# Kernel optimization log

Measured on AMD Instinct MI355X. Metric: run time of the kernel, lower is better.

The kernel has to match this reference:

```python
import jax, jax.numpy as jnp
import numpy as np

B, S, V, D, H, C, NH = 8, 512, 32000, 768, 768, 9, 8
DH = D // NH


def setup_inputs() -> dict:
    key = jax.random.key(0)
    ks = list(jax.random.split(key, 24))
    it = iter(ks)

    def w(shape, s=0.02):
        return jax.random.normal(next(it), shape, jnp.float32) * s

    return {
        "input_ids": jax.random.randint(next(it), (B, S), 0, V, dtype=jnp.int32),
        "labels": jax.random.randint(next(it), (B, S), 0, C, dtype=jnp.int32),
        "emb_table": w((V, D), 1.0),
        "hw_Wh": w((D, D)),
        "hw_bh": jnp.zeros((D,), jnp.float32),
        "hw_Wt": w((D, D)),
        "hw_bt": jnp.zeros((D,), jnp.float32),
        "in_proj_w": w((3 * D, D)),
        "in_proj_b": jnp.zeros((3 * D,), jnp.float32),
        "out_proj_w": w((D, D)),
        "out_proj_b": jnp.zeros((D,), jnp.float32),
        "lstm0_Wih": w((2, 4 * H, D)),
        "lstm0_Whh": w((2, 4 * H, H)),
        "lstm0_b": jnp.zeros((2, 4 * H), jnp.float32),
        "lstm1_Wih": w((2, 4 * H, 2 * H)),
        "lstm1_Whh": w((2, 4 * H, H)),
        "lstm1_b": jnp.zeros((2, 4 * H), jnp.float32),
        "fc_W": w((C, 2 * H)),
        "fc_b": jnp.zeros((C,), jnp.float32),
        "crf_start": w((C,), 0.1),
        "crf_end": w((C,), 0.1),
        "crf_trans": w((C, C), 0.1),
    }


def _lstm_dir(x, Wih, Whh, b, reverse):
    # x: [B,S,in] -> outputs [B,S,H]; PyTorch gate order i,f,g,o
    xt = x.transpose(1, 0, 2)  # [S,B,in]
    h0 = jnp.zeros((x.shape[0], H), x.dtype)

    def step(carry, xt_):
        h, c = carry
        g = xt_ @ Wih.T + h @ Whh.T + b
        i, f, gg, o = jnp.split(g, 4, axis=-1)
        c = jax.nn.sigmoid(f) * c + jax.nn.sigmoid(i) * jnp.tanh(gg)
        h = jax.nn.sigmoid(o) * jnp.tanh(c)
        return (h, c), h

    _, hs = jax.lax.scan(step, (h0, h0), xt, reverse=reverse)
    return hs.transpose(1, 0, 2)


def _bilstm_layer(x, Wih, Whh, b):
    fwd = _lstm_dir(x, Wih[0], Whh[0], b[0], False)
    bwd = _lstm_dir(x, Wih[1], Whh[1], b[1], True)
    return jnp.concatenate([fwd, bwd], axis=-1)


def _emissions(input_ids, emb_table, hw_Wh, hw_bh, hw_Wt, hw_bt,
               in_proj_w, in_proj_b, out_proj_w, out_proj_b,
               lstm0_Wih, lstm0_Whh, lstm0_b, lstm1_Wih, lstm1_Whh, lstm1_b,
               fc_W, fc_b):
    x = emb_table[input_ids]  # [B,S,D]
    # Highway (1 layer, relu)
    hh = jax.nn.relu(x @ hw_Wh.T + hw_bh)
    t = jax.nn.sigmoid(x @ hw_Wt.T + hw_bt)
    x = t * hh + (1.0 - t) * x
    # Multi-head self-attention
    qkv = x @ in_proj_w.T + in_proj_b
    q, k, v = jnp.split(qkv, 3, axis=-1)
    hd = lambda a: a.reshape(B, S, NH, DH).transpose(0, 2, 1, 3)  # [B,NH,S,DH]
    q, k, v = hd(q), hd(k), hd(v)
    att = jax.nn.softmax(jnp.einsum('bhqd,bhkd->bhqk', q, k) / np.float32(np.sqrt(DH)), axis=-1)
    o = jnp.einsum('bhqk,bhkd->bhqd', att, v).transpose(0, 2, 1, 3).reshape(B, S, D)
    x = o @ out_proj_w.T + out_proj_b
    # 2-layer BiLSTM (inference: dropout off)
    x = _bilstm_layer(x, lstm0_Wih, lstm0_Whh, lstm0_b)
    x = _bilstm_layer(x, lstm1_Wih, lstm1_Whh, lstm1_b)
    return x @ fc_W.T + fc_b  # [B,S,C]


def _crf_nll(emissions, tags, crf_start, crf_end, crf_trans):
    # full mask (labels==-100 replaced by 0 before mask built), reduction='sum'
    em_t = emissions.transpose(1, 0, 2)  # [S,B,C]
    num = crf_start[tags[:, 0]] + crf_end[tags[:, -1]]
    num = num + jnp.take_along_axis(emissions, tags[..., None], axis=-1)[..., 0].sum(-1)
    num = num + crf_trans[tags[:, :-1], tags[:, 1:]].sum(-1)
    a0 = crf_start + em_t[0]  # [B,C]

    def fstep(a, em):
        a = jax.scipy.special.logsumexp(a[:, :, None] + crf_trans[None], axis=1) + em
        return a, None

    aT, _ = jax.lax.scan(fstep, a0, em_t[1:])
    logZ = jax.scipy.special.logsumexp(aT + crf_end, axis=-1)
    return -(num - logZ).sum()


def _viterbi(emissions, crf_start, crf_end, crf_trans):
    em_t = emissions.transpose(1, 0, 2)  # [S,B,C]
    s0 = crf_start + em_t[0]

    def vstep(s, em):
        sc = s[:, :, None] + crf_trans[None]  # [B,C_prev,C_next]
        return jnp.max(sc, axis=1) + em, jnp.argmax(sc, axis=1)

    sT, bps = jax.lax.scan(vstep, s0, em_t[1:])  # bps: [S-1,B,C]
    last = jnp.argmax(sT + crf_end, axis=-1)  # [B]

    def bstep(tag, bp):
        prev = jnp.take_along_axis(bp, tag[:, None], axis=1)[:, 0]
        return prev, prev

    _, path = jax.lax.scan(bstep, last, bps, reverse=True)  # [S-1,B]
    return jnp.concatenate([path, last[None]], axis=0).transpose(1, 0)  # [B,S]


def reference(input_ids, labels, emb_table, hw_Wh, hw_bh, hw_Wt, hw_bt,
              in_proj_w, in_proj_b, out_proj_w, out_proj_b,
              lstm0_Wih, lstm0_Whh, lstm0_b, lstm1_Wih, lstm1_Whh, lstm1_b,
              fc_W, fc_b, crf_start, crf_end, crf_trans):
    emissions = _emissions(input_ids, emb_table, hw_Wh, hw_bh, hw_Wt, hw_bt,
                           in_proj_w, in_proj_b, out_proj_w, out_proj_b,
                           lstm0_Wih, lstm0_Whh, lstm0_b,
                           lstm1_Wih, lstm1_Whh, lstm1_b, fc_W, fc_b)
    loss = _crf_nll(emissions, labels, crf_start, crf_end, crf_trans)
    decode = _viterbi(emissions, crf_start, crf_end, crf_trans)
    return loss, decode
```

## Files before the change

kernel.cpp:

```cpp
#include <hip/hip_runtime.h>
#include <cstdint>

#define B_   8
#define S_   512
#define D_   768
#define C_   9
#define BS_  4096

typedef unsigned long long u64;

__global__ __launch_bounds__(192) void k_embed(const int* __restrict__ ids,
                                               const float* __restrict__ emb,
                                               float* __restrict__ x) {
  int row = blockIdx.x;
  int id = ids[row];
  const float4* src = (const float4*)(emb + (size_t)id * D_);
  float4* dst = (float4*)(x + (size_t)row * D_);
  dst[threadIdx.x] = src[threadIdx.x];
}

#define GIDX(k, m) ((k)*144 + (m) + (((m) >> 5) << 2))

__global__ __launch_bounds__(256) void k_gemm(const float* __restrict__ A,
                                              const float* __restrict__ W,
                                              const float* __restrict__ bias,
                                              float* __restrict__ C,
                                              int M, int N, int K, int act, int mode) {
  __shared__ float As[2304];
  __shared__ float Bs[2304];
  int bm0 = blockIdx.y * 128, bn0 = blockIdx.x * 128;
  int tid = threadIdx.x;
  int tm = tid >> 4, tn = tid & 15;
  float acc[8][8];
#pragma unroll
  for (int i = 0; i < 8; ++i)
#pragma unroll
    for (int j = 0; j < 8; ++j) acc[i][j] = 0.f;

  for (int k0 = 0; k0 < K; k0 += 16) {
    __syncthreads();
#pragma unroll
    for (int j = 0; j < 2; ++j) {
      int f4 = tid + j * 256;
      int r = f4 >> 2;
      int kq = (f4 & 3) * 4;
      float4 va = *(const float4*)(A + (size_t)(bm0 + r) * K + k0 + kq);
      As[GIDX(kq + 0, r)] = va.x; As[GIDX(kq + 1, r)] = va.y;
      As[GIDX(kq + 2, r)] = va.z; As[GIDX(kq + 3, r)] = va.w;
      float4 vb = *(const float4*)(W + (size_t)(bn0 + r) * K + k0 + kq);
      Bs[GIDX(kq + 0, r)] = vb.x; Bs[GIDX(kq + 1, r)] = vb.y;
      Bs[GIDX(kq + 2, r)] = vb.z; Bs[GIDX(kq + 3, r)] = vb.w;
    }
    __syncthreads();
#pragma unroll
    for (int kk = 0; kk < 16; ++kk) {
      float a[8], b[8];
      *(float4*)&a[0] = *(const float4*)&As[GIDX(kk, tm * 8)];
      *(float4*)&a[4] = *(const float4*)&As[GIDX(kk, tm * 8 + 4)];
      *(float4*)&b[0] = *(const float4*)&Bs[GIDX(kk, tn * 8)];
      *(float4*)&b[4] = *(const float4*)&Bs[GIDX(kk, tn * 8 + 4)];
#pragma unroll
      for (int i = 0; i < 8; ++i)
#pragma unroll
        for (int j = 0; j < 8; ++j) acc[i][j] += a[i] * b[j];
    }
  }

  float bv[8];
#pragma unroll
  for (int j = 0; j < 8; ++j) bv[j] = bias[bn0 + tn * 8 + j];
#pragma unroll
  for (int i = 0; i < 8; ++i) {
    int row = bm0 + tm * 8 + i;
    float o[8];
#pragma unroll
    for (int j = 0; j < 8; ++j) {
      float v = acc[i][j] + bv[j];
      if (act == 1) v = fmaxf(v, 0.f);
      else if (act == 2) v = 1.f / (1.f + expf(-v));
      o[j] = v;
    }
    if (mode == 0) {
      float* cp = C + (size_t)row * N + bn0 + tn * 8;
      *(float4*)cp = make_float4(o[0], o[1], o[2], o[3]);
      *(float4*)(cp + 4) = make_float4(o[4], o[5], o[6], o[7]);
    } else {
      int bb = row >> 9, t = row & 511;
#pragma unroll
      for (int j = 0; j < 8; ++j) {
        unsigned n = bn0 + tn * 8 + j;
        unsigned dir = n / 3072u;
        unsigned n2 = n - dir * 3072u;
        unsigned g = n2 / 768u;
        unsigned rem = n2 - g * 768u;
        unsigned grp = rem >> 3, u = rem & 7;
        C[(((size_t)(dir * 512 + t) * 96 + grp) << 8) + u * 32 + g * 8 + bb] = o[j];
      }
    }
  }
}

__global__ __launch_bounds__(256) void k_highway(float* __restrict__ x,
                                                 const float* __restrict__ hh,
                                                 const float* __restrict__ tt) {
  const int n4 = BS_ * D_ / 4;
  for (int i = blockIdx.x * 256 + threadIdx.x; i < n4; i += gridDim.x * 256) {
    float4 xv = ((const float4*)x)[i];
    float4 hv = ((const float4*)hh)[i];
    float4 tv = ((const float4*)tt)[i];
    xv.x = tv.x * hv.x + (1.f - tv.x) * xv.x;
    xv.y = tv.y * hv.y + (1.f - tv.y) * xv.y;
    xv.z = tv.z * hv.z + (1.f - tv.z) * xv.z;
    xv.w = tv.w * hv.w + (1.f - tv.w) * xv.w;
    ((float4*)x)[i] = xv;
  }
}

__global__ __launch_bounds__(256) void k_attn(const float* __restrict__ qkv,
                                              float* __restrict__ out) {
  __shared__ float Qs[16 * 100];
  __shared__ float Ks[32 * 101];
  __shared__ float Ps[16 * 513];
  int bh = blockIdx.x;
  int b = bh >> 3, h = bh & 7;
  int q0 = blockIdx.y * 16;
  int tid = threadIdx.x;
  const float scale = 0.10206207261596577f;

  const float* qb = qkv + (size_t)(b * 512 + q0) * 2304 + h * 96;
  for (int i = tid; i < 16 * 96; i += 256) {
    int r = i / 96, c = i - r * 96;
    Qs[r * 100 + c] = qb[(size_t)r * 2304 + c];
  }
  int qi = tid >> 4, kseg = tid & 15;

  for (int kt = 0; kt < 16; ++kt) {
    __syncthreads();
    const float* kb = qkv + (size_t)(b * 512 + kt * 32) * 2304 + 768 + h * 96;
    for (int i = tid; i < 32 * 96; i += 256) {
      int r = i / 96, c = i - r * 96;
      Ks[r * 101 + c] = kb[(size_t)r * 2304 + c];
    }
    __syncthreads();
    int kj0 = kseg * 2;
    float s0 = 0.f, s1 = 0.f;
    const float* qrow = &Qs[qi * 100];
    const float* k0p = &Ks[kj0 * 101];
    const float* k1p = &Ks[(kj0 + 1) * 101];
#pragma unroll 8
    for (int d = 0; d < 96; ++d) {
      float qv = qrow[d];
      s0 += qv * k0p[d];
      s1 += qv * k1p[d];
    }
    Ps[qi * 513 + kt * 32 + kj0] = s0 * scale;
    Ps[qi * 513 + kt * 32 + kj0 + 1] = s1 * scale;
  }
  __syncthreads();

  {
    float m = -1e30f;
    for (int j = 0; j < 32; ++j) m = fmaxf(m, Ps[qi * 513 + kseg + j * 16]);
    m = fmaxf(m, __shfl_xor(m, 1)); m = fmaxf(m, __shfl_xor(m, 2));
    m = fmaxf(m, __shfl_xor(m, 4)); m = fmaxf(m, __shfl_xor(m, 8));
    float sum = 0.f;
    for (int j = 0; j < 32; ++j) {
      int idx = qi * 513 + kseg + j * 16;
      float e = expf(Ps[idx] - m);
      Ps[idx] = e;
      sum += e;
    }
    sum += __shfl_xor(sum, 1); sum += __shfl_xor(sum, 2);
    sum += __shfl_xor(sum, 4); sum += __shfl_xor(sum, 8);
    float inv = 1.f / sum;
    for (int j = 0; j < 32; ++j) Ps[qi * 513 + kseg + j * 16] *= inv;
  }

  float acc[6] = {0.f, 0.f, 0.f, 0.f, 0.f, 0.f};
  int d0 = kseg * 6;
  for (int kt = 0; kt < 16; ++kt) {
    __syncthreads();
    const float* vb = qkv + (size_t)(b * 512 + kt * 32) * 2304 + 1536 + h * 96;
    for (int i = tid; i < 32 * 96; i += 256) {
      int r = i / 96, c = i - r * 96;
      Ks[r * 101 + c] = vb[(size_t)r * 2304 + c];
    }
    __syncthreads();
#pragma unroll 4
    for (int kj = 0; kj < 32; ++kj) {
      float p = Ps[qi * 513 + kt * 32 + kj];
      const float* vrow = &Ks[kj * 101 + d0];
#pragma unroll
      for (int u = 0; u < 6; ++u) acc[u] += p * vrow[u];
    }
  }
  float* ob = out + (size_t)(b * 512 + q0 + qi) * 768 + h * 96 + d0;
#pragma unroll
  for (int u = 0; u < 6; ++u) ob[u] = acc[u];
}

#define NWGD 96
__global__ __launch_bounds__(256, 1) void k_lstm(const float* __restrict__ gates,
                                                 const float* __restrict__ Whh,
                                                 float* __restrict__ hbuf,
                                                 float* __restrict__ hs,
                                                 int* __restrict__ flags) {
  __shared__ float hlds[8 * 772];
  int tid = threadIdx.x;
  int wg = blockIdx.x;
  int dir = wg / NWGD;
  int grp = wg % NWGD;
  int rg = tid >> 5;
  int ks = tid & 31;

  float4 w4[4][6];
#pragma unroll
  for (int j = 0; j < 4; ++j) {
    const float* wp = Whh + ((size_t)dir * 3072 + j * 768 + grp * 8 + rg) * 768 + ks * 4;
#pragma unroll
    for (int jj = 0; jj < 6; ++jj)
      w4[j][jj] = *(const float4*)(wp + jj * 128);
  }

  float* hb = hbuf + (size_t)dir * 2 * 6144;
  const float* gbase = gates + (size_t)dir * 512 * 24576 + grp * 256 + tid;
  int* barp = flags;
  float cst = 0.f;
  const float* hp = hlds + ks * 4;

  for (int step = 0; step < 512; ++step) {
    int t = dir ? (511 - step) : step;
    float gqv = gbase[(size_t)t * 24576];

#pragma unroll
    for (int i = 0; i < 3; ++i) {
      int idx = i * 256 + tid;
      int b2 = idx / 96;
      int kq = (idx - b2 * 96) * 8;
      const u64* src = (const u64*)(hb + (step & 1) * 6144 + b2 * 768 + kq);
      u64 lo = __hip_atomic_load(src + 0, __ATOMIC_RELAXED, __HIP_MEMORY_SCOPE_AGENT);
      u64 hi = __hip_atomic_load(src + 1, __ATOMIC_RELAXED, __HIP_MEMORY_SCOPE_AGENT);
      u64 lo2 = __hip_atomic_load(src + 2, __ATOMIC_RELAXED, __HIP_MEMORY_SCOPE_AGENT);
      u64 hi2 = __hip_atomic_load(src + 3, __ATOMIC_RELAXED, __HIP_MEMORY_SCOPE_AGENT);
      float* dst = &hlds[b2 * 772 + kq];
      *(u64*)(dst + 0) = lo;
      *(u64*)(dst + 2) = hi;
      *(u64*)(dst + 4) = lo2;
      *(u64*)(dst + 6) = hi2;
    }
    __syncthreads();

    float v[32];
#pragma unroll
    for (int i = 0; i < 32; ++i) v[i] = 0.f;
#pragma unroll
    for (int jj = 0; jj < 6; ++jj) {
#pragma unroll
      for (int b2 = 0; b2 < 8; ++b2) {
        float4 hv = *(const float4*)(hp + b2 * 772 + jj * 128);
#pragma unroll
        for (int j = 0; j < 4; ++j) {
          float4 w = w4[j][jj];
          v[j * 8 + b2] = fmaf(w.x, hv.x, v[j * 8 + b2]);
          v[j * 8 + b2] = fmaf(w.y, hv.y, v[j * 8 + b2]);
          v[j * 8 + b2] = fmaf(w.z, hv.z, v[j * 8 + b2]);
          v[j * 8 + b2] = fmaf(w.w, hv.w, v[j * 8 + b2]);
        }
      }
    }

    {
      bool hi = (ks & 16) != 0;
#pragma unroll
      for (int i = 0; i < 16; ++i) {
        float keep = hi ? v[i + 16] : v[i];
        float send = hi ? v[i] : v[i + 16];
        v[i] = keep + __shfl_xor(send, 16);
      }
    }
    {
      bool hi = (ks & 8) != 0;
#pragma unroll
      for (int i = 0; i < 8; ++i) {
        float keep = hi ? v[i + 8] : v[i];
        float send = hi ? v[i] : v[i + 8];
        v[i] = keep + __shfl_xor(send, 8);
      }
    }
    {
      bool hi = (ks & 4) != 0;
#pragma unroll
      for (int i = 0; i < 4; ++i) {
        float keep = hi ? v[i + 4] : v[i];
        float send = hi ? v[i] : v[i + 4];
        v[i] = keep + __shfl_xor(send, 4);
      }
    }
    {
      bool hi = (ks & 2) != 0;
#pragma unroll
      for (int i = 0; i < 2; ++i) {
        float keep = hi ? v[i + 2] : v[i];
        float send = hi ? v[i] : v[i + 2];
        v[i] = keep + __shfl_xor(send, 2);
      }
    }
    {
      bool hi = (ks & 1) != 0;
      float keep = hi ? v[1] : v[0];
      float send = hi ? v[0] : v[1];
      v[0] = keep + __shfl_xor(send, 1);
    }

    float gv = v[0] + gqv;
    float gf = __shfl_down(gv, 8);
    float gg = __shfl_down(gv, 16);
    float go = __shfl_down(gv, 24);
    if (ks < 8) {
      float i_ = 1.f / (1.f + expf(-gv));
      float f_ = 1.f / (1.f + expf(-gf));
      float ci = tanhf(gg);
      float o_ = 1.f / (1.f + expf(-go));
      cst = f_ * cst + i_ * ci;
      float hnew = o_ * tanhf(cst);
      int hidden = grp * 8 + rg;
      __hip_atomic_store(hb + ((step + 1) & 1) * 6144 + ks * 768 + hidden, hnew,
                         __ATOMIC_RELAXED, __HIP_MEMORY_SCOPE_AGENT);
      hs[((size_t)(ks * 512 + t)) * 1536 + dir * 768 + hidden] = hnew;
    }

    __syncthreads();
    if (tid == 0)
      __hip_atomic_store(&barp[wg * 32], step + 1, __ATOMIC_RELAXED, __HIP_MEMORY_SCOPE_AGENT);
    if (tid < NWGD) {
      const int* fp = &barp[(dir * NWGD + tid) * 32];
      while (__hip_atomic_load(fp, __ATOMIC_RELAXED, __HIP_MEMORY_SCOPE_AGENT) <= step)
        __builtin_amdgcn_s_sleep(2);
    }
    __syncthreads();
  }
}

__global__ __launch_bounds__(256) void k_fc(const float* __restrict__ A,
                                            const float* __restrict__ Wf,
                                            const float* __restrict__ bf,
                                            float* __restrict__ out) {
  __shared__ float Wl[9 * 1536];
  int tid = threadIdx.x;
  for (int i = tid; i < 9 * 1536; i += 256) Wl[i] = Wf[i];
  __syncthreads();
  int lane = tid & 63, wv = tid >> 6;
  int row = blockIdx.x * 4 + wv;
  const float* a = A + (size_t)row * 1536;
  float acc[9];
#pragma unroll
  for (int c = 0; c < 9; ++c) acc[c] = 0.f;
  for (int i = 0; i < 24; ++i) {
    float av = a[lane + i * 64];
#pragma unroll
    for (int c = 0; c < 9; ++c) acc[c] += av * Wl[c * 1536 + lane + i * 64];
  }
#pragma unroll
  for (int c = 0; c < 9; ++c) {
#pragma unroll
    for (int m = 1; m < 64; m <<= 1) acc[c] += __shfl_xor(acc[c], m);
  }
  if (lane == 0) {
#pragma unroll
    for (int c = 0; c < 9; ++c) out[(size_t)row * 9 + c] = acc[c] + bf[c];
  }
}

__global__ __launch_bounds__(128) void k_crf(const float* __restrict__ em,
                                             const int* __restrict__ labels,
                                             const float* __restrict__ cs,
                                             const float* __restrict__ ce,
                                             const float* __restrict__ ct,
                                             float* __restrict__ out) {
  __shared__ float trans[9][12];
  __shared__ float ab[2][8][9];
  __shared__ float vb[2][8][9];
  __shared__ unsigned char bps[511][8][9];
  __shared__ float red[128];
  __shared__ float lz[8];
  int tid = threadIdx.x;
  if (tid < 81) trans[tid / 9][tid % 9] = ct[tid];
  if (tid < 72) {
    int b = tid / 9, c = tid % 9;
    float v = cs[c] + em[(b * 512) * 9 + c];
    ab[0][b][c] = v;
    vb[0][b][c] = v;
  }
  __syncthreads();
  for (int t = 1; t < 512; ++t) {
    int rp = (t - 1) & 1, wp = t & 1;
    if (tid < 72) {
      int b = tid / 9, cn = tid % 9;
      float e = em[(b * 512 + t) * 9 + cn];
      float m = -1e30f, vm = -1e30f;
      int bp = 0;
#pragma unroll
      for (int cp = 0; cp < 9; ++cp) {
        float x = ab[rp][b][cp] + trans[cp][cn];
        m = fmaxf(m, x);
        float y = vb[rp][b][cp] + trans[cp][cn];
        if (y > vm) { vm = y; bp = cp; }
      }
      float ssum = 0.f;
#pragma unroll
      for (int cp = 0; cp < 9; ++cp)
        ssum += expf(ab[rp][b][cp] + trans[cp][cn] - m);
      ab[wp][b][cn] = m + logf(ssum) + e;
      vb[wp][b][cn] = vm + e;
      bps[t - 1][b][cn] = (unsigned char)bp;
    }
    __syncthreads();
  }
  float part = 0.f;
  for (int idx = tid; idx < 4096; idx += 128) {
    int b = idx >> 9, t = idx & 511;
    int tg = labels[b * 512 + t];
    part += em[(b * 512 + t) * 9 + tg];
    if (t < 511) part += trans[tg][labels[b * 512 + t + 1]];
  }
  if (tid < 8) part += cs[labels[tid * 512]] + ce[labels[tid * 512 + 511]];
  red[tid] = part;
  __syncthreads();
  for (int s2 = 64; s2 > 0; s2 >>= 1) {
    if (tid < s2) red[tid] += red[tid + s2];
    __syncthreads();
  }
  if (tid < 8) {
    int b = tid;
    float m = -1e30f;
#pragma unroll
    for (int c = 0; c < 9; ++c) m = fmaxf(m, ab[1][b][c] + ce[c]);
    float ssum = 0.f;
#pragma unroll
    for (int c = 0; c < 9; ++c) ssum += expf(ab[1][b][c] + ce[c] - m);
    lz[b] = m + logf(ssum);
  }
  __syncthreads();
  if (tid == 0) {
    float z = 0.f;
#pragma unroll
    for (int b = 0; b < 8; ++b) z += lz[b];
    out[0] = -(red[0] - z);
  }
  if (tid < 8) {
    int b = tid;
    float bv2 = vb[1][b][0] + ce[0];
    int best = 0;
#pragma unroll
    for (int c = 1; c < 9; ++c) {
      float y = vb[1][b][c] + ce[c];
      if (y > bv2) { bv2 = y; best = c; }
    }
    out[1 + b * 512 + 511] = (float)best;
    int tg = best;
    for (int t = 510; t >= 0; --t) {
      tg = bps[t][b][tg];
      out[1 + b * 512 + t] = (float)tg;
    }
  }
}

extern "C" void kernel_launch(void* const* d_in, const int* in_sizes, int n_in,
                              void* d_out, int out_size, void* d_ws, size_t ws_size,
                              hipStream_t stream) {
  (void)in_sizes; (void)n_in; (void)out_size; (void)ws_size;
  const int*   ids    = (const int*)d_in[0];
  const int*   labels = (const int*)d_in[1];
  const float* emb    = (const float*)d_in[2];
  const float* hwWh   = (const float*)d_in[3];
  const float* hwbh   = (const float*)d_in[4];
  const float* hwWt   = (const float*)d_in[5];
  const float* hwbt   = (const float*)d_in[6];
  const float* ipw    = (const float*)d_in[7];
  const float* ipb    = (const float*)d_in[8];
  const float* opw    = (const float*)d_in[9];
  const float* opb    = (const float*)d_in[10];
  const float* l0Wih  = (const float*)d_in[11];
  const float* l0Whh  = (const float*)d_in[12];
  const float* l0b    = (const float*)d_in[13];
  const float* l1Wih  = (const float*)d_in[14];
  const float* l1Whh  = (const float*)d_in[15];
  const float* l1b    = (const float*)d_in[16];
  const float* fcW    = (const float*)d_in[17];
  const float* fcb    = (const float*)d_in[18];
  const float* cs     = (const float*)d_in[19];
  const float* ce     = (const float*)d_in[20];
  const float* ct     = (const float*)d_in[21];

  float* ws   = (float*)d_ws;
  float* x0   = ws;
  float* gbuf = ws + 3145728;
  float* hh   = gbuf;
  float* tt   = gbuf + 3145728;
  float* qkv  = gbuf + 6291456;
  float* x1   = ws + 28311552;
  float* hs0  = ws + 31457280;
  float* hs1  = ws + 37748736;
  float* em   = ws + 44040192;
  float* hbuf = ws + 44077056;
  int*   flags = (int*)(ws + 44101632);

  dim3 g768(6, 32), g2304(18, 32), g6144(48, 32);

  k_embed<<<BS_, 192, 0, stream>>>(ids, emb, x0);
  k_gemm<<<g768, 256, 0, stream>>>(x0, hwWh, hwbh, hh, BS_, 768, 768, 1, 0);
  k_gemm<<<g768, 256, 0, stream>>>(x0, hwWt, hwbt, tt, BS_, 768, 768, 2, 0);
  k_highway<<<768, 256, 0, stream>>>(x0, hh, tt);
  k_gemm<<<g2304, 256, 0, stream>>>(x0, ipw, ipb, qkv, BS_, 2304, 768, 0, 0);
  k_attn<<<dim3(64, 32), 256, 0, stream>>>(qkv, x0);
  k_gemm<<<g768, 256, 0, stream>>>(x0, opw, opb, x1, BS_, 768, 768, 0, 0);

  k_gemm<<<g6144, 256, 0, stream>>>(x1, l0Wih, l0b, gbuf, BS_, 6144, 768, 0, 1);
  hipMemsetAsync(hbuf, 0, (24576 + 192 * 32) * sizeof(float), stream);
  k_lstm<<<192, 256, 0, stream>>>(gbuf, l0Whh, hbuf, hs0, flags);

  k_gemm<<<g6144, 256, 0, stream>>>(hs0, l1Wih, l1b, gbuf, BS_, 6144, 1536, 0, 1);
  hipMemsetAsync(hbuf, 0, (24576 + 192 * 32) * sizeof(float), stream);
  k_lstm<<<192, 256, 0, stream>>>(gbuf, l1Whh, hbuf, hs1, flags);

  k_fc<<<1024, 256, 0, stream>>>(hs1, fcW, fcb, em);
  k_crf<<<1, 128, 0, stream>>>(em, labels, cs, ce, ct, (float*)d_out);
}
```

Baseline: 8.109 ms.

## Restructure LSTM step sync: poll flags before h load, stage outputs in LDS

```diff
diff --git a/kernel.cpp b/kernel.cpp
--- a/kernel.cpp
+++ b/kernel.cpp
@@ -206,6 +206,7 @@
                                                  float* __restrict__ hs,
                                                  int* __restrict__ flags) {
   __shared__ float hlds[8 * 772];
+  __shared__ float hout[64];
   int tid = threadIdx.x;
   int wg = blockIdx.x;
   int dir = wg / NWGD;
@@ -224,31 +225,50 @@
 
   float* hb = hbuf + (size_t)dir * 2 * 6144;
   const float* gbase = gates + (size_t)dir * 512 * 24576 + grp * 256 + tid;
-  int* barp = flags;
+  const float* hp = hlds + ks * 4;
   float cst = 0.f;
-  const float* hp = hlds + ks * 4;
+
+  const int* fp0 = &flags[((size_t)dir * NWGD + (unsigned)((tid +   0) % 192) / 2) * 32];
+  const int* fp1 = &flags[((size_t)dir * NWGD + (unsigned)((tid +  64) % 192) / 2) * 32];
+  const int* fp2 = &flags[((size_t)dir * NWGD + (unsigned)((tid + 128) % 192) / 2) * 32];
+  int* myflag = &flags[(size_t)wg * 32];
+
+  int t0 = dir ? 511 : 0;
+  float gq = gbase[(size_t)t0 * 24576];
 
   for (int step = 0; step < 512; ++step) {
     int t = dir ? (511 - step) : step;
-    float gqv = gbase[(size_t)t * 24576];
-
-#pragma unroll
-    for (int i = 0; i < 3; ++i) {
-      int idx = i * 256 + tid;
-      int b2 = idx / 96;
-      int kq = (idx - b2 * 96) * 8;
-      const u64* src = (const u64*)(hb + (step & 1) * 6144 + b2 * 768 + kq);
-      u64 lo = __hip_atomic_load(src + 0, __ATOMIC_RELAXED, __HIP_MEMORY_SCOPE_AGENT);
-      u64 hi = __hip_atomic_load(src + 1, __ATOMIC_RELAXED, __HIP_MEMORY_SCOPE_AGENT);
-      u64 lo2 = __hip_atomic_load(src + 2, __ATOMIC_RELAXED, __HIP_MEMORY_SCOPE_AGENT);
-      u64 hi2 = __hip_atomic_load(src + 3, __ATOMIC_RELAXED, __HIP_MEMORY_SCOPE_AGENT);
-      float* dst = &hlds[b2 * 772 + kq];
-      *(u64*)(dst + 0) = lo;
-      *(u64*)(dst + 2) = hi;
-      *(u64*)(dst + 4) = lo2;
-      *(u64*)(dst + 6) = hi2;
-    }
-    __syncthreads();
+
+    for (;;) {
+      int f0 = __hip_atomic_load(fp0, __ATOMIC_RELAXED, __HIP_MEMORY_SCOPE_AGENT);
+      int f1 = __hip_atomic_load(fp1, __ATOMIC_RELAXED, __HIP_MEMORY_SCOPE_AGENT);
+      int f2 = __hip_atomic_load(fp2, __ATOMIC_RELAXED, __HIP_MEMORY_SCOPE_AGENT);
+      if (f0 >= step && f1 >= step && f2 >= step) break;
+      __builtin_amdgcn_s_sleep(1);
+    }
+
+    {
+      const float* hsrc = hb + (step & 1) * 6144;
+#pragma unroll
+      for (int i = 0; i < 6; ++i) {
+        int idx = i * 256 + tid;
+        int b2 = idx / 192;
+        int r4 = (idx - b2 * 192) * 4;
+        const u64* src = (const u64*)(hsrc + b2 * 768 + r4);
+        u64 lo = __hip_atomic_load(src + 0, __ATOMIC_RELAXED, __HIP_MEMORY_SCOPE_AGENT);
+        u64 hi = __hip_atomic_load(src + 1, __ATOMIC_RELAXED, __HIP_MEMORY_SCOPE_AGENT);
+        float* dst = &hlds[b2 * 772 + r4];
+        *(u64*)(dst + 0) = lo;
+        *(u64*)(dst + 2) = hi;
+      }
+    }
+    __syncthreads();
+
+    float gq_next = 0.f;
+    if (step < 511) {
+      int tn = dir ? (t - 1) : (t + 1);
+      gq_next = gbase[(size_t)tn * 24576];
+    }
 
     float v[32];
 #pragma unroll
@@ -312,7 +332,8 @@
       v[0] = keep + __shfl_xor(send, 1);
     }
 
-    float gv = v[0] + gqv;
+    float gv = v[0] + gq;
+    gq = gq_next;
     float gf = __shfl_down(gv, 8);
     float gg = __shfl_down(gv, 16);
     float go = __shfl_down(gv, 24);
@@ -323,21 +344,25 @@
       float o_ = 1.f / (1.f + expf(-go));
       cst = f_ * cst + i_ * ci;
       float hnew = o_ * tanhf(cst);
-      int hidden = grp * 8 + rg;
-      __hip_atomic_store(hb + ((step + 1) & 1) * 6144 + ks * 768 + hidden, hnew,
-                         __ATOMIC_RELAXED, __HIP_MEMORY_SCOPE_AGENT);
-      hs[((size_t)(ks * 512 + t)) * 1536 + dir * 768 + hidden] = hnew;
-    }
-
-    __syncthreads();
-    if (tid == 0)
-      __hip_atomic_store(&barp[wg * 32], step + 1, __ATOMIC_RELAXED, __HIP_MEMORY_SCOPE_AGENT);
-    if (tid < NWGD) {
-      const int* fp = &barp[(dir * NWGD + tid) * 32];
-      while (__hip_atomic_load(fp, __ATOMIC_RELAXED, __HIP_MEMORY_SCOPE_AGENT) <= step)
-        __builtin_amdgcn_s_sleep(2);
-    }
-    __syncthreads();
+      hout[ks * 8 + rg] = hnew;
+    }
+    __syncthreads();
+
+    if (tid < 32) {
+      int bb = tid >> 2, qq = tid & 3;
+      u64 val = *(const u64*)&hout[tid * 2];
+      __hip_atomic_store((u64*)(hb + ((step + 1) & 1) * 6144 + bb * 768 + grp * 8 + qq * 2),
+                         val, __ATOMIC_RELAXED, __HIP_MEMORY_SCOPE_AGENT);
+    }
+    if (tid == 0) {
+      asm volatile("s_waitcnt vmcnt(0)" ::: "memory");
+      __hip_atomic_store(myflag, step + 1, __ATOMIC_RELAXED, __HIP_MEMORY_SCOPE_AGENT);
+    }
+    if (tid >= 64 && tid < 80) {
+      int l = tid - 64, bb = l >> 1, half = l & 1;
+      *(float4*)&hs[((size_t)(bb * 512 + t)) * 1536 + dir * 768 + grp * 8 + half * 4] =
+          *(const float4*)&hout[bb * 8 + half * 4];
+    }
   }
 }
 
```

Result: slower. 8.870 ms (+9.4%).

## Interleave both LSTM directions per workgroup with ping-pong grid barriers

Applied to the files above, without the earlier changes.

```diff
diff --git a/kernel.cpp b/kernel.cpp
--- a/kernel.cpp
+++ b/kernel.cpp
@@ -89,12 +89,11 @@
 #pragma unroll
       for (int j = 0; j < 8; ++j) {
         unsigned n = bn0 + tn * 8 + j;
-        unsigned dir = n / 3072u;
-        unsigned n2 = n - dir * 3072u;
+        unsigned d = n / 3072u;
+        unsigned n2 = n - d * 3072u;
         unsigned g = n2 / 768u;
-        unsigned rem = n2 - g * 768u;
-        unsigned grp = rem >> 3, u = rem & 7;
-        C[(((size_t)(dir * 512 + t) * 96 + grp) << 8) + u * 32 + g * 8 + bb] = o[j];
+        unsigned u = n2 - g * 768u;
+        C[(((size_t)(d * 512 + t) * 768 + u) << 5) + g * 8 + bb] = o[j];
       }
     }
   }
@@ -199,145 +198,246 @@
   for (int u = 0; u < 6; ++u) ob[u] = acc[u];
 }
 
-#define NWGD 96
+#define NWG 192
 __global__ __launch_bounds__(256, 1) void k_lstm(const float* __restrict__ gates,
                                                  const float* __restrict__ Whh,
                                                  float* __restrict__ hbuf,
                                                  float* __restrict__ hs,
                                                  int* __restrict__ flags) {
-  __shared__ float hlds[8 * 772];
+  __shared__ float hlds0[8 * 772];
+  __shared__ float hlds1[8 * 772];
   int tid = threadIdx.x;
-  int wg = blockIdx.x;
-  int dir = wg / NWGD;
-  int grp = wg % NWGD;
-  int rg = tid >> 5;
-  int ks = tid & 31;
-
-  float4 w4[4][6];
+  int wg  = blockIdx.x;
+  int rg  = tid >> 6;
+  int lane = tid & 63;
+  int unit = wg * 4 + rg;
+  int idx = (lane >> 1) & 31;
+  bool owner = ((lane & 1) == 0) && (lane < 16);
+  int bb = lane >> 1;
+
+  float4 w0[4][3], w1[4][3];
 #pragma unroll
   for (int j = 0; j < 4; ++j) {
-    const float* wp = Whh + ((size_t)dir * 3072 + j * 768 + grp * 8 + rg) * 768 + ks * 4;
-#pragma unroll
-    for (int jj = 0; jj < 6; ++jj)
-      w4[j][jj] = *(const float4*)(wp + jj * 128);
-  }
-
-  float* hb = hbuf + (size_t)dir * 2 * 6144;
-  const float* gbase = gates + (size_t)dir * 512 * 24576 + grp * 256 + tid;
-  int* barp = flags;
-  float cst = 0.f;
-  const float* hp = hlds + ks * 4;
+    const float* p0 = Whh + ((size_t)(j * 768 + unit)) * 768 + lane * 4;
+    const float* p1 = Whh + ((size_t)(3072 + j * 768 + unit)) * 768 + lane * 4;
+#pragma unroll
+    for (int jj = 0; jj < 3; ++jj) {
+      w0[j][jj] = *(const float4*)(p0 + jj * 256);
+      w1[j][jj] = *(const float4*)(p1 + jj * 256);
+    }
+  }
+
+  float* hb0 = hbuf;
+  float* hb1 = hbuf + 2 * 6144;
+  int* f0 = flags;
+  int* f1 = flags + NWG * 8;
+  const float* gbase = gates + (size_t)unit * 32 + idx;
+
+  float cst0 = 0.f, cst1 = 0.f;
+  float gq0 = gbase[0];
+  float gq1 = gbase[(size_t)1023 * 24576];
 
   for (int step = 0; step < 512; ++step) {
-    int t = dir ? (511 - step) : step;
-    float gqv = gbase[(size_t)t * 24576];
-
-#pragma unroll
-    for (int i = 0; i < 3; ++i) {
-      int idx = i * 256 + tid;
-      int b2 = idx / 96;
-      int kq = (idx - b2 * 96) * 8;
-      const u64* src = (const u64*)(hb + (step & 1) * 6144 + b2 * 768 + kq);
-      u64 lo = __hip_atomic_load(src + 0, __ATOMIC_RELAXED, __HIP_MEMORY_SCOPE_AGENT);
-      u64 hi = __hip_atomic_load(src + 1, __ATOMIC_RELAXED, __HIP_MEMORY_SCOPE_AGENT);
-      u64 lo2 = __hip_atomic_load(src + 2, __ATOMIC_RELAXED, __HIP_MEMORY_SCOPE_AGENT);
-      u64 hi2 = __hip_atomic_load(src + 3, __ATOMIC_RELAXED, __HIP_MEMORY_SCOPE_AGENT);
-      float* dst = &hlds[b2 * 772 + kq];
-      *(u64*)(dst + 0) = lo;
-      *(u64*)(dst + 2) = hi;
-      *(u64*)(dst + 4) = lo2;
-      *(u64*)(dst + 6) = hi2;
-    }
-    __syncthreads();
-
-    float v[32];
-#pragma unroll
-    for (int i = 0; i < 32; ++i) v[i] = 0.f;
-#pragma unroll
-    for (int jj = 0; jj < 6; ++jj) {
-#pragma unroll
-      for (int b2 = 0; b2 < 8; ++b2) {
-        float4 hv = *(const float4*)(hp + b2 * 772 + jj * 128);
-#pragma unroll
-        for (int j = 0; j < 4; ++j) {
-          float4 w = w4[j][jj];
-          v[j * 8 + b2] = fmaf(w.x, hv.x, v[j * 8 + b2]);
-          v[j * 8 + b2] = fmaf(w.y, hv.y, v[j * 8 + b2]);
-          v[j * 8 + b2] = fmaf(w.z, hv.z, v[j * 8 + b2]);
-          v[j * 8 + b2] = fmaf(w.w, hv.w, v[j * 8 + b2]);
-        }
-      }
-    }
-
+    int t = step, t1 = 511 - step;
+    float gq0n = 0.f, gq1n = 0.f;
+    if (step < 511) {
+      gq0n = gbase[(size_t)(t + 1) * 24576];
+      gq1n = gbase[(size_t)(1022 - step) * 24576];
+    }
+
+    if (tid < NWG) {
+      const int* fp = &f0[tid * 8];
+      while (__hip_atomic_load(fp, __ATOMIC_RELAXED, __HIP_MEMORY_SCOPE_AGENT) < step)
+        __builtin_amdgcn_s_sleep(2);
+    }
     {
-      bool hi = (ks & 16) != 0;
-#pragma unroll
-      for (int i = 0; i < 16; ++i) {
-        float keep = hi ? v[i + 16] : v[i];
-        float send = hi ? v[i] : v[i + 16];
-        v[i] = keep + __shfl_xor(send, 16);
-      }
-    }
+      const float* hsrc = hb0 + (step & 1) * 6144;
+#pragma unroll
+      for (int i = 0; i < 6; ++i) {
+        int id2 = i * 256 + tid;
+        int b2 = id2 / 192;
+        int r4 = (id2 - b2 * 192) * 4;
+        const u64* src = (const u64*)(hsrc + b2 * 768 + r4);
+        u64 lo = __hip_atomic_load(src,     __ATOMIC_RELAXED, __HIP_MEMORY_SCOPE_AGENT);
+        u64 hi = __hip_atomic_load(src + 1, __ATOMIC_RELAXED, __HIP_MEMORY_SCOPE_AGENT);
+        float* dst = &hlds0[b2 * 772 + r4];
+        *(u64*)dst = lo; *(u64*)(dst + 2) = hi;
+      }
+    }
+    __syncthreads();
+    if (tid == 0)
+      __hip_atomic_store(&f1[wg * 8], step, __ATOMIC_RELAXED, __HIP_MEMORY_SCOPE_AGENT);
+
     {
-      bool hi = (ks & 8) != 0;
-#pragma unroll
-      for (int i = 0; i < 8; ++i) {
-        float keep = hi ? v[i + 8] : v[i];
-        float send = hi ? v[i] : v[i + 8];
-        v[i] = keep + __shfl_xor(send, 8);
-      }
+      const float* hp = hlds0 + lane * 4;
+      float v[32];
+#pragma unroll
+      for (int i = 0; i < 32; ++i) v[i] = 0.f;
+#pragma unroll
+      for (int jj = 0; jj < 3; ++jj)
+#pragma unroll
+        for (int b2 = 0; b2 < 8; ++b2) {
+          float4 hv = *(const float4*)(hp + b2 * 772 + jj * 256);
+#pragma unroll
+          for (int j = 0; j < 4; ++j) {
+            float4 w = w0[j][jj];
+            v[j * 8 + b2] = fmaf(w.x, hv.x, v[j * 8 + b2]);
+            v[j * 8 + b2] = fmaf(w.y, hv.y, v[j * 8 + b2]);
+            v[j * 8 + b2] = fmaf(w.z, hv.z, v[j * 8 + b2]);
+            v[j * 8 + b2] = fmaf(w.w, hv.w, v[j * 8 + b2]);
+          }
+        }
+      {
+        bool hi = (lane & 32) != 0;
+#pragma unroll
+        for (int i = 0; i < 16; ++i) {
+          float keep = hi ? v[i + 16] : v[i], send = hi ? v[i] : v[i + 16];
+          v[i] = keep + __shfl_xor(send, 32);
+        }
+      }
+      {
+        bool hi = (lane & 16) != 0;
+#pragma unroll
+        for (int i = 0; i < 8; ++i) {
+          float keep = hi ? v[i + 8] : v[i], send = hi ? v[i] : v[i + 8];
+          v[i] = keep + __shfl_xor(send, 16);
+        }
+      }
+      {
+        bool hi = (lane & 8) != 0;
+#pragma unroll
+        for (int i = 0; i < 4; ++i) {
+          float keep = hi ? v[i + 4] : v[i], send = hi ? v[i] : v[i + 4];
+          v[i] = keep + __shfl_xor(send, 8);
+        }
+      }
+      {
+        bool hi = (lane & 4) != 0;
+#pragma unroll
+        for (int i = 0; i < 2; ++i) {
+          float keep = hi ? v[i + 2] : v[i], send = hi ? v[i] : v[i + 2];
+          v[i] = keep + __shfl_xor(send, 4);
+        }
+      }
+      {
+        bool hi = (lane & 2) != 0;
+        float keep = hi ? v[1] : v[0], send = hi ? v[0] : v[1];
+        v[0] = keep + __shfl_xor(send, 2);
+      }
+      float gv = v[0] + gq0;
+      gq0 = gq0n;
+      float gf = __shfl_down(gv, 16);
+      float gg = __shfl_down(gv, 32);
+      float go = __shfl_down(gv, 48);
+      if (owner) {
+        float i_ = 1.f / (1.f + expf(-gv));
+        float f_ = 1.f / (1.f + expf(-gf));
+        float ci = tanhf(gg);
+        float o_ = 1.f / (1.f + expf(-go));
+        cst0 = f_ * cst0 + i_ * ci;
+        float hnew = o_ * tanhf(cst0);
+        __hip_atomic_store(hb0 + ((step + 1) & 1) * 6144 + bb * 768 + unit, hnew,
+                           __ATOMIC_RELAXED, __HIP_MEMORY_SCOPE_AGENT);
+        hs[((size_t)(bb * 512 + t)) * 1536 + unit] = hnew;
+      }
+    }
+
+    if (tid < NWG) {
+      const int* fp = &f1[tid * 8];
+      while (__hip_atomic_load(fp, __ATOMIC_RELAXED, __HIP_MEMORY_SCOPE_AGENT) < step)
+        __builtin_amdgcn_s_sleep(2);
     }
     {
-      bool hi = (ks & 4) != 0;
-#pragma unroll
-      for (int i = 0; i < 4; ++i) {
-        float keep = hi ? v[i + 4] : v[i];
-        float send = hi ? v[i] : v[i + 4];
-        v[i] = keep + __shfl_xor(send, 4);
-      }
-    }
+      const float* hsrc = hb1 + (step & 1) * 6144;
+#pragma unroll
+      for (int i = 0; i < 6; ++i) {
+        int id2 = i * 256 + tid;
+        int b2 = id2 / 192;
+        int r4 = (id2 - b2 * 192) * 4;
+        const u64* src = (const u64*)(hsrc + b2 * 768 + r4);
+        u64 lo = __hip_atomic_load(src,     __ATOMIC_RELAXED, __HIP_MEMORY_SCOPE_AGENT);
+        u64 hi = __hip_atomic_load(src + 1, __ATOMIC_RELAXED, __HIP_MEMORY_SCOPE_AGENT);
+        float* dst = &hlds1[b2 * 772 + r4];
+        *(u64*)dst = lo; *(u64*)(dst + 2) = hi;
+      }
+    }
+    __syncthreads();
+    if (tid == 0)
+      __hip_atomic_store(&f0[wg * 8], step + 1, __ATOMIC_RELAXED, __HIP_MEMORY_SCOPE_AGENT);
+
     {
-      bool hi = (ks & 2) != 0;
-#pragma unroll
-      for (int i = 0; i < 2; ++i) {
-        float keep = hi ? v[i + 2] : v[i];
-        float send = hi ? v[i] : v[i + 2];
-        v[i] = keep + __shfl_xor(send, 2);
-      }
-    }
-    {
-      bool hi = (ks & 1) != 0;
-      float keep = hi ? v[1] : v[0];
-      float send = hi ? v[0] : v[1];
-      v[0] = keep + __shfl_xor(send, 1);
-    }
-
-    float gv = v[0] + gqv;
-    float gf = __shfl_down(gv, 8);
-    float gg = __shfl_down(gv, 16);
-    float go = __shfl_down(gv, 24);
-    if (ks < 8) {
-      float i_ = 1.f / (1.f + expf(-gv));
-      float f_ = 1.f / (1.f + expf(-gf));
-      float ci = tanhf(gg);
-      float o_ = 1.f / (1.f + expf(-go));
-      cst = f_ * cst + i_ * ci;
-      float hnew = o_ * tanhf(cst);
-      int hidden = grp * 8 + rg;
-      __hip_atomic_store(hb + ((step + 1) & 1) * 6144 + ks * 768 + hidden, hnew,
-                         __ATOMIC_RELAXED, __HIP_MEMORY_SCOPE_AGENT);
-      hs[((size_t)(ks * 512 + t)) * 1536 + dir * 768 + hidden] = hnew;
-    }
-
-    __syncthreads();
-    if (tid == 0)
-      __hip_atomic_store(&barp[wg * 32], step + 1, __ATOMIC_RELAXED, __HIP_MEMORY_SCOPE_AGENT);
-    if (tid < NWGD) {
-      const int* fp = &barp[(dir * NWGD + tid) * 32];
-      while (__hip_atomic_load(fp, __ATOMIC_RELAXED, __HIP_MEMORY_SCOPE_AGENT) <= step)
-        __builtin_amdgcn_s_sleep(2);
-    }
-    __syncthreads();
+      const float* hp = hlds1 + lane * 4;
+      float v[32];
+#pragma unroll
+      for (int i = 0; i < 32; ++i) v[i] = 0.f;
+#pragma unroll
+      for (int jj = 0; jj < 3; ++jj)
+#pragma unroll
+        for (int b2 = 0; b2 < 8; ++b2) {
+          float4 hv = *(const float4*)(hp + b2 * 772 + jj * 256);
+#pragma unroll
+          for (int j = 0; j < 4; ++j) {
+            float4 w = w1[j][jj];
+            v[j * 8 + b2] = fmaf(w.x, hv.x, v[j * 8 + b2]);
+            v[j * 8 + b2] = fmaf(w.y, hv.y, v[j * 8 + b2]);
+            v[j * 8 + b2] = fmaf(w.z, hv.z, v[j * 8 + b2]);
+            v[j * 8 + b2] = fmaf(w.w, hv.w, v[j * 8 + b2]);
+          }
+        }
+      {
+        bool hi = (lane & 32) != 0;
+#pragma unroll
+        for (int i = 0; i < 16; ++i) {
+          float keep = hi ? v[i + 16] : v[i], send = hi ? v[i] : v[i + 16];
+          v[i] = keep + __shfl_xor(send, 32);
+        }
+      }
+      {
+        bool hi = (lane & 16) != 0;
+#pragma unroll
+        for (int i = 0; i < 8; ++i) {
+          float keep = hi ? v[i + 8] : v[i], send = hi ? v[i] : v[i + 8];
+          v[i] = keep + __shfl_xor(send, 16);
+        }
+      }
+      {
+        bool hi = (lane & 8) != 0;
+#pragma unroll
+        for (int i = 0; i < 4; ++i) {
+          float keep = hi ? v[i + 4] : v[i], send = hi ? v[i] : v[i + 4];
+          v[i] = keep + __shfl_xor(send, 8);
+        }
+      }
+      {
+        bool hi = (lane & 4) != 0;
+#pragma unroll
+        for (int i = 0; i < 2; ++i) {
+          float keep = hi ? v[i + 2] : v[i], send = hi ? v[i] : v[i + 2];
+          v[i] = keep + __shfl_xor(send, 4);
+        }
+      }
+      {
+        bool hi = (lane & 2) != 0;
+        float keep = hi ? v[1] : v[0], send = hi ? v[0] : v[1];
+        v[0] = keep + __shfl_xor(send, 2);
+      }
+      float gv = v[0] + gq1;
+      gq1 = gq1n;
+      float gf = __shfl_down(gv, 16);
+      float gg = __shfl_down(gv, 32);
+      float go = __shfl_down(gv, 48);
+      if (owner) {
+        float i_ = 1.f / (1.f + expf(-gv));
+        float f_ = 1.f / (1.f + expf(-gf));
+        float ci = tanhf(gg);
+        float o_ = 1.f / (1.f + expf(-go));
+        cst1 = f_ * cst1 + i_ * ci;
+        float hnew = o_ * tanhf(cst1);
+        __hip_atomic_store(hb1 + ((step + 1) & 1) * 6144 + bb * 768 + unit, hnew,
+                           __ATOMIC_RELAXED, __HIP_MEMORY_SCOPE_AGENT);
+        hs[((size_t)(bb * 512 + t1)) * 1536 + 768 + unit] = hnew;
+      }
+    }
   }
 }
 
@@ -516,12 +616,12 @@
   k_gemm<<<g768, 256, 0, stream>>>(x0, opw, opb, x1, BS_, 768, 768, 0, 0);
 
   k_gemm<<<g6144, 256, 0, stream>>>(x1, l0Wih, l0b, gbuf, BS_, 6144, 768, 0, 1);
-  hipMemsetAsync(hbuf, 0, (24576 + 192 * 32) * sizeof(float), stream);
-  k_lstm<<<192, 256, 0, stream>>>(gbuf, l0Whh, hbuf, hs0, flags);
+  hipMemsetAsync(hbuf, 0, (24576 + 2 * NWG * 8) * sizeof(float), stream);
+  k_lstm<<<NWG, 256, 0, stream>>>(gbuf, l0Whh, hbuf, hs0, flags);
 
   k_gemm<<<g6144, 256, 0, stream>>>(hs0, l1Wih, l1b, gbuf, BS_, 6144, 1536, 0, 1);
-  hipMemsetAsync(hbuf, 0, (24576 + 192 * 32) * sizeof(float), stream);
-  k_lstm<<<192, 256, 0, stream>>>(gbuf, l1Whh, hbuf, hs1, flags);
+  hipMemsetAsync(hbuf, 0, (24576 + 2 * NWG * 8) * sizeof(float), stream);
+  k_lstm<<<NWG, 256, 0, stream>>>(gbuf, l1Whh, hbuf, hs1, flags);
 
   k_fc<<<1024, 256, 0, stream>>>(hs1, fcW, fcb, em);
   k_crf<<<1, 128, 0, stream>>>(em, labels, cs, ce, ct, (float*)d_out);
```

Result: slower. 10.64 ms (+31.2%).
